# Optimization experiments

Measured on AMD Instinct MI355X. Metric: run time of the kernel, lower is better.

The kernel has to match this reference:

```python
import jax, jax.numpy as jnp
import numpy as np

B, T, D, U = 128, 1024, 256, 256


def setup_inputs() -> dict:
    key = jax.random.key(0)
    ks = jax.random.split(key, 16)
    s_in = 1.0 / np.sqrt(D)
    s_rec = 1.0 / np.sqrt(U)
    inp = {"x": jax.random.normal(ks[0], (B, T, D), dtype=jnp.float32)}
    for i, name in enumerate(["wf", "wi", "wc", "wo"]):
        inp[name] = jax.random.normal(ks[1 + i], (D, U), dtype=jnp.float32) * s_in
    for i, name in enumerate(["rf", "ri", "rc", "ro", "pf", "pi", "po"]):
        inp[name] = jax.random.normal(ks[5 + i], (U, U), dtype=jnp.float32) * s_rec
    for i, name in enumerate(["bf", "bi", "bc", "bo"]):
        inp[name] = jax.random.normal(ks[12 + i], (U,), dtype=jnp.float32) * 0.01
    return inp


def reference(x, wf, wi, wc, wo, rf, ri, rc, ro, pf, pi, po, bf, bi, bc, bo):
    # Peephole LSTM: scan over time, state (c, h) each [B, U].
    def step(carry, xt):
        c, h = carry
        f_gate = jax.nn.sigmoid(xt @ wf + h @ rf + c @ pf + bf)
        i_gate = jax.nn.sigmoid(xt @ wi + h @ ri + c @ pi + bi)
        c_tild = jnp.tanh(xt @ wc + h @ rc + bc)
        c_new = f_gate * c + i_gate * c_tild
        o_gate = jax.nn.sigmoid(xt @ wo + h @ ro + c_new @ po + bo)
        h_new = jnp.tanh(c_new) * o_gate
        return (c_new, h_new), None

    b = x.shape[0]
    u = wf.shape[1]
    c0 = jnp.zeros((b, u), dtype=x.dtype)
    h0 = jnp.zeros((b, u), dtype=x.dtype)
    (_, h_final), _ = jax.lax.scan(step, (c0, h0), jnp.swapaxes(x, 0, 1))  # time-major [T,B,D]
    return h_final
```

## Files before the change

kernel.cpp:

```cpp
#include <hip/hip_runtime.h>

#define TT 1024
#define DU 256

#define CEX_OFF   0
#define HEX_OFF   65536
#define STMP_OFF  131072
#define TST_OFF   139264
#define GCON_OFF  172032
#define BLOB_OFF  174080
#define CHUNK_ELEMS (11*16*256)

typedef unsigned short ushort_t;
typedef unsigned u32;
typedef unsigned long long u64;
typedef __attribute__((ext_vector_type(8))) short short8;
typedef __attribute__((ext_vector_type(2))) unsigned long long u64x2;
typedef __attribute__((ext_vector_type(4))) float floatx4;

#define MFMA(a, b, c) __builtin_amdgcn_mfma_f32_16x16x32_bf16((a), (b), (c), 0, 0, 0)

__device__ __forceinline__ ushort_t f2bf(float f) {
  unsigned u = __float_as_uint(f);
  return (ushort_t)((u + 0x7fffu + ((u >> 16) & 1u)) >> 16);
}
__device__ __forceinline__ float sigf(float x) { return 1.0f / (1.0f + __expf(-x)); }
__device__ __forceinline__ float tanhf_(float x) {
  float t = 1.0f - 2.0f / (__expf(2.0f * fabsf(x)) + 1.0f);
  return copysignf(t, x);
}

__device__ __forceinline__ short8 ldfrag(const ushort_t* p) {
  union { struct { u64 a, b; } q; short8 s; } v;
  v.q.a = __hip_atomic_load((const u64*)p,       __ATOMIC_RELAXED, __HIP_MEMORY_SCOPE_AGENT);
  v.q.b = __hip_atomic_load((const u64*)(p + 4), __ATOMIC_RELAXED, __HIP_MEMORY_SCOPE_AGENT);
  return v.s;
}
__device__ __forceinline__ void wait_half_slow(const u32* stG, u32 tgt, int lane, int wv) {
  const u32* p = stG + (wv * 8 + (lane & 7)) * 2 + ((lane >> 3) & 1);
  for (;;) {
    u32 s = __hip_atomic_load(p, __ATOMIC_RELAXED, __HIP_MEMORY_SCOPE_AGENT);
    if (__all((int)(s >= tgt))) return;
    __builtin_amdgcn_s_sleep(1);
  }
}

__device__ __forceinline__ u32 poll_nt(const u32* p) {
  u32 s;
  asm volatile("global_load_dword %0, %1, off nt\n\ts_waitcnt vmcnt(0)"
               : "=v"(s) : "v"(p) : "memory");
  return s;
}
__device__ __forceinline__ int wait_half_f(const u32* stG, u32 tgt, int lane, int wv) {
  const u32* p = stG + (wv * 8 + (lane & 7)) * 2 + ((lane >> 3) & 1);
  int it = 0;
  for (;;) {
    u32 s = poll_nt(p);
    if (__all((int)(s >= tgt))) return 1;
    if (++it > 16384) return 0;
  }
}
__device__ __forceinline__ short8 ldfrag_nt(const ushort_t* p) {
  union { u64x2 q; short8 s; } v;
  v.q = __builtin_nontemporal_load((const u64x2*)p);
  return v.s;
}

__device__ int test_nt(u32* tb, int mem, int lane) {
  u64* td = (u64*)tb;
  u32* tstamp = tb + 256;
  u32* tready = tb + 512;
  int ok = 1;
  for (int r = 0; r < 3; ++r) {
    u32 seq = 1u + (u32)r;
    if (lane == 0)
      __hip_atomic_store(tready + mem, seq, __ATOMIC_RELEASE, __HIP_MEMORY_SCOPE_AGENT);
    { int it = 0;
      for (;;) {
        u32 v = __hip_atomic_load(tready + (lane & 15), __ATOMIC_RELAXED,
                                  __HIP_MEMORY_SCOPE_AGENT);
        if (__all((int)(v >= seq))) break;
        if (++it > 16384) return 0;
        __builtin_amdgcn_s_sleep(2);
      } }
    if (lane < 8) {
      u64 v = 0x9E3779B97F4A7C15ull * (u64)(seq * 131u + (u32)mem * 17u + (u32)lane + 1u);
      asm volatile("global_store_dwordx2 %0, %1, off"
                   :: "v"(td + mem * 8 + lane), "v"(v) : "memory");
    }
    asm volatile("s_waitcnt vmcnt(0)" ::: "memory");
    if (lane == 0)
      asm volatile("global_store_dword %0, %1, off"
                   :: "v"(tstamp + mem * 16), "v"(seq) : "memory");
    int saw = 0;
    { int it = 0;
      for (;;) {
        u32 s = poll_nt(tstamp + (lane & 15) * 16);
        if (__all((int)(s >= seq))) { saw = 1; break; }
        if (++it > 192) break;
        __builtin_amdgcn_s_sleep(2);
      } }
    if (!saw) { ok = 0; continue; }
    u64 a = __builtin_nontemporal_load(td + lane);
    u64 b = __builtin_nontemporal_load(td + lane + 64);
    int s0 = lane >> 3, j0 = lane & 7, s1 = (lane + 64) >> 3, j1 = (lane + 64) & 7;
    u64 e0 = 0x9E3779B97F4A7C15ull * (u64)(seq * 131u + (u32)s0 * 17u + (u32)j0 + 1u);
    u64 e1 = 0x9E3779B97F4A7C15ull * (u64)(seq * 131u + (u32)s1 * 17u + (u32)j1 + 1u);
    if (!__all((int)((a == e0) && (b == e1)))) ok = 0;
  }
  return ok;
}

__global__ void conv_weights(
    const float* __restrict__ wf, const float* __restrict__ wi,
    const float* __restrict__ wc, const float* __restrict__ wo,
    const float* __restrict__ rf, const float* __restrict__ ri,
    const float* __restrict__ rc, const float* __restrict__ ro,
    const float* __restrict__ pf, const float* __restrict__ pi,
    const float* __restrict__ po, ushort_t* __restrict__ blob)
{
  int id = blockIdx.x * 256 + threadIdx.x;
  int k   = id & 255;
  int col = (id >> 8) & 15;
  int q   = id >> 12;
  int m   = q % 11;
  int mm  = q / 11;
  const float* srcs[11] = {wf, wi, wc, wo, rf, ri, rc, ro, pf, pi, po};
  float v = srcs[m][k * 256 + mm * 16 + col];
  unsigned u = __float_as_uint(v);
  blob[id] = (ushort_t)((u + 0x7fffu + ((u >> 16) & 1u)) >> 16);
}

extern "C" __global__ void __launch_bounds__(128, 1)
lstm_rec(const float* __restrict__ x, const ushort_t* __restrict__ blob,
         ushort_t* __restrict__ h_ex, ushort_t* __restrict__ c_ex,
         u32* __restrict__ stamps, u32* __restrict__ tst, u32* __restrict__ gcon,
         const float* __restrict__ bfv, const float* __restrict__ biv,
         const float* __restrict__ bcv, const float* __restrict__ bov,
         float* __restrict__ out)
{
  __shared__ ushort_t xa[16 * 264];
  __shared__ float pre2[2][4][16][17];
  __shared__ float pop2[2][16][17];
  __shared__ float bia[4][16];
  __shared__ int s_mode;

  const int tid = threadIdx.x;
  const int bid = blockIdx.x;
  const int wv = tid >> 6;
  const int lane = tid & 63;
  const int lr = lane & 15;
  const int lk = lane >> 4;

  const int grp = bid & 7;
  const int mem = bid >> 3;
  const int gb0 = grp * 16;
  const int gc0 = mem * 16;

  u32* gok  = gcon;
  u32* gpol = gcon + 256;

  if (wv == 0) {
    __builtin_amdgcn_fence(__ATOMIC_ACQUIRE, "agent");
    int okv = test_nt(tst + grp * 1024, mem, lane);
    if (lane == 0)
      __hip_atomic_store(gok + bid, 1u | ((u32)okv << 1),
                         __ATOMIC_RELEASE, __HIP_MEMORY_SCOPE_AGENT);
    if (bid == 0) {
      u32 pol = 0; int it = 0;
      for (;;) {
        u32 a = __hip_atomic_load(gok + lane, __ATOMIC_RELAXED, __HIP_MEMORY_SCOPE_AGENT);
        u32 b = __hip_atomic_load(gok + 64 + lane, __ATOMIC_RELAXED, __HIP_MEMORY_SCOPE_AGENT);
        if (__all((int)((a & 1u) && (b & 1u)))) {
          pol = __all((int)(((a >> 1) & 1u) && ((b >> 1) & 1u))) ? 1u : 0u;
          break;
        }
        if (++it > 32768) { pol = 0; break; }
        __builtin_amdgcn_s_sleep(4);
      }
      if (lane == 0)
        __hip_atomic_store(gpol, pol + 1u, __ATOMIC_RELEASE, __HIP_MEMORY_SCOPE_AGENT);
    }
    u32 p;
    for (;;) {
      p = __hip_atomic_load(gpol, __ATOMIC_RELAXED, __HIP_MEMORY_SCOPE_AGENT);
      if (p) break;
      __builtin_amdgcn_s_sleep(4);
    }
    if (lane == 0) s_mode = (int)(p - 1u);
  }
  __syncthreads();
  const int mode = s_mode;
  int wedged = 0;
  if (mode) __builtin_amdgcn_fence(__ATOMIC_ACQUIRE, "agent");

  const ushort_t* wb = blob + (size_t)mem * CHUNK_ELEMS;
  short8 wW[4][4], wR[4][4], wPf[4], wPi[4], wPo[4];
#pragma unroll
  for (int s = 0; s < 4; ++s) {
    const int ko = wv * 128 + s * 32 + lk * 8;
#pragma unroll
    for (int g = 0; g < 4; ++g) {
      wW[g][s] = *(const short8*)(wb + ((g    ) * 16 + lr) * 256 + ko);
      wR[g][s] = *(const short8*)(wb + ((4 + g) * 16 + lr) * 256 + ko);
    }
    wPf[s] = *(const short8*)(wb + (8  * 16 + lr) * 256 + ko);
    wPi[s] = *(const short8*)(wb + (9  * 16 + lr) * 256 + ko);
    wPo[s] = *(const short8*)(wb + (10 * 16 + lr) * 256 + ko);
  }

  if (tid < 64) {
    const float* bs = (tid < 16) ? bfv : (tid < 32) ? biv : (tid < 48) ? bcv : bov;
    bia[tid >> 4][tid & 15] = bs[gc0 + (tid & 15)];
  }
  const int pb = tid >> 3, pc = (tid & 7) * 2;
  float cr0 = 0.f, cr1 = 0.f;

  const int xr = tid >> 3, xc = (tid & 7) * 32;
  {
    const float* xp = x + (size_t)(gb0 + xr) * TT * DU + xc;
#pragma unroll
    for (int u = 0; u < 8; ++u) {
      float4 f = *(const float4*)(xp + u * 4);
      *(u64*)&xa[xr * 264 + xc + u * 4] =
          (u64)f2bf(f.x) | ((u64)f2bf(f.y) << 16) |
          ((u64)f2bf(f.z) << 32) | ((u64)f2bf(f.w) << 48);
    }
  }
  __syncthreads();

  const floatx4 z4 = {0.f, 0.f, 0.f, 0.f};
  floatx4 acc[4] = {z4, z4, z4, z4};
#pragma unroll
  for (int s = 0; s < 4; ++s) {
    int k = wv * 128 + s * 32 + lk * 8;
    short8 a = *(const short8*)&xa[lr * 264 + k];
    acc[0] = MFMA(a, wW[0][s], acc[0]);
    acc[1] = MFMA(a, wW[1][s], acc[1]);
    acc[2] = MFMA(a, wW[2][s], acc[2]);
    acc[3] = MFMA(a, wW[3][s], acc[3]);
  }

  u32* stG = stamps + grp * 32;
  ushort_t* cG = c_ex + grp * 16 * 256;
  ushort_t* hG = h_ex + grp * 16 * 256;
  u32* cSlot = (u32*)(cG + mem * 256 + pb * 16 + pc);
  u32* hSlot = (u32*)(hG + mem * 256 + pb * 16 + pc);
  u32* mySt  = stG + mem * 2 + wv;

  for (int t = 0; t < TT; ++t) {
    if (t > 0) {
      if (mode) { if (!wedged && !wait_half_f(stG, 2u * (u32)t, lane, wv)) wedged = 1; }
      else wait_half_slow(stG, 2u * (u32)t, lane, wv);
      short8 hf[4];
#pragma unroll
      for (int s = 0; s < 4; ++s) {
        int k = wv * 128 + s * 32 + lk * 8;
        hf[s] = mode ? ldfrag_nt(hG + (k >> 4) * 256 + lr * 16 + (k & 15))
                     : ldfrag(hG + (k >> 4) * 256 + lr * 16 + (k & 15));
      }
#pragma unroll
      for (int s = 0; s < 4; ++s) {
        acc[0] = MFMA(hf[s], wR[0][s], acc[0]);
        acc[1] = MFMA(hf[s], wR[1][s], acc[1]);
        acc[2] = MFMA(hf[s], wR[2][s], acc[2]);
        acc[3] = MFMA(hf[s], wR[3][s], acc[3]);
      }
    }
#pragma unroll
    for (int g = 0; g < 4; ++g)
#pragma unroll
      for (int r = 0; r < 4; ++r)
        pre2[wv][g][lk * 4 + r][lr] = acc[g][r];
    __syncthreads();

    {
      float fg = sigf(pre2[0][0][pb][pc] + pre2[1][0][pb][pc] + bia[0][pc]);
      float ig = sigf(pre2[0][1][pb][pc] + pre2[1][1][pb][pc] + bia[1][pc]);
      float ct = tanhf_(pre2[0][2][pb][pc] + pre2[1][2][pb][pc] + bia[2][pc]);
      cr0 = fg * cr0 + ig * ct;
      fg = sigf(pre2[0][0][pb][pc + 1] + pre2[1][0][pb][pc + 1] + bia[0][pc + 1]);
      ig = sigf(pre2[0][1][pb][pc + 1] + pre2[1][1][pb][pc + 1] + bia[1][pc + 1]);
      ct = tanhf_(pre2[0][2][pb][pc + 1] + pre2[1][2][pb][pc + 1] + bia[2][pc + 1]);
      cr1 = fg * cr1 + ig * ct;
    }
    {
      u32 cw = (u32)f2bf(cr0) | ((u32)f2bf(cr1) << 16);
      if (mode)
        asm volatile("global_store_dword %0, %1, off" :: "v"(cSlot), "v"(cw) : "memory");
      else
        __hip_atomic_store(cSlot, cw, __ATOMIC_RELAXED, __HIP_MEMORY_SCOPE_AGENT);
      asm volatile("s_waitcnt vmcnt(0)" ::: "memory");
      if (lane == 0) {
        u32 sv = 2u * (u32)t + 1u;
        if (mode)
          asm volatile("global_store_dword %0, %1, off" :: "v"(mySt), "v"(sv) : "memory");
        else
          __hip_atomic_store(mySt, sv, __ATOMIC_RELAXED, __HIP_MEMORY_SCOPE_AGENT);
      }
    }

    if (t < TT - 1) {
      float4 xf[8];
      const float* xp = x + ((size_t)(gb0 + xr) * TT + (t + 1)) * DU + xc;
#pragma unroll
      for (int u = 0; u < 8; ++u) xf[u] = *(const float4*)(xp + u * 4);
#pragma unroll
      for (int u = 0; u < 8; ++u) {
        float4 f = xf[u];
        *(u64*)&xa[xr * 264 + xc + u * 4] =
            (u64)f2bf(f.x) | ((u64)f2bf(f.y) << 16) |
            ((u64)f2bf(f.z) << 32) | ((u64)f2bf(f.w) << 48);
      }
      __syncthreads();
    }

    if (mode) { if (!wedged && !wait_half_f(stG, 2u * (u32)t + 1u, lane, wv)) wedged = 1; }
    else wait_half_slow(stG, 2u * (u32)t + 1u, lane, wv);

    short8 cf[4];
#pragma unroll
    for (int s = 0; s < 4; ++s) {
      int k = wv * 128 + s * 32 + lk * 8;
      cf[s] = mode ? ldfrag_nt(cG + (k >> 4) * 256 + lr * 16 + (k & 15))
                   : ldfrag(cG + (k >> 4) * 256 + lr * 16 + (k & 15));
    }
    {
      floatx4 pacc = z4;
#pragma unroll
      for (int s = 0; s < 4; ++s) pacc = MFMA(cf[s], wPo[s], pacc);
#pragma unroll
      for (int r = 0; r < 4; ++r) pop2[wv][lk * 4 + r][lr] = pacc[r];
    }
    __syncthreads();

    float og0 = sigf(pre2[0][3][pb][pc] + pre2[1][3][pb][pc]
                   + pop2[0][pb][pc] + pop2[1][pb][pc] + bia[3][pc]);
    float hv0 = tanhf_(cr0) * og0;
    float og1 = sigf(pre2[0][3][pb][pc + 1] + pre2[1][3][pb][pc + 1]
                   + pop2[0][pb][pc + 1] + pop2[1][pb][pc + 1] + bia[3][pc + 1]);
    float hv1 = tanhf_(cr1) * og1;
    if (t == TT - 1) {
      float2 o2; o2.x = hv0; o2.y = hv1;
      *(float2*)&out[(gb0 + pb) * 256 + gc0 + pc] = o2;
      break;
    }
    {
      u32 hw = (u32)f2bf(hv0) | ((u32)f2bf(hv1) << 16);
      if (mode)
        asm volatile("global_store_dword %0, %1, off" :: "v"(hSlot), "v"(hw) : "memory");
      else
        __hip_atomic_store(hSlot, hw, __ATOMIC_RELAXED, __HIP_MEMORY_SCOPE_AGENT);
      asm volatile("s_waitcnt vmcnt(0)" ::: "memory");
      if (lane == 0) {
        u32 sv = 2u * (u32)t + 2u;
        if (mode)
          asm volatile("global_store_dword %0, %1, off" :: "v"(mySt), "v"(sv) : "memory");
        else
          __hip_atomic_store(mySt, sv, __ATOMIC_RELAXED, __HIP_MEMORY_SCOPE_AGENT);
      }
    }

#pragma unroll
    for (int g = 0; g < 4; ++g) acc[g] = z4;
#pragma unroll
    for (int s = 0; s < 4; ++s) {
      int k = wv * 128 + s * 32 + lk * 8;
      short8 a = *(const short8*)&xa[lr * 264 + k];
      acc[0] = MFMA(a, wW[0][s], acc[0]);
      acc[1] = MFMA(a, wW[1][s], acc[1]);
      acc[2] = MFMA(a, wW[2][s], acc[2]);
      acc[3] = MFMA(a, wW[3][s], acc[3]);
    }
#pragma unroll
    for (int s = 0; s < 4; ++s) {
      acc[0] = MFMA(cf[s], wPf[s], acc[0]);
      acc[1] = MFMA(cf[s], wPi[s], acc[1]);
    }
  }
}

extern "C" void kernel_launch(void* const* d_in, const int* in_sizes, int n_in,
                              void* d_out, int out_size, void* d_ws, size_t ws_size,
                              hipStream_t stream) {
  const float* x   = (const float*)d_in[0];
  const float* bfv = (const float*)d_in[12];
  const float* biv = (const float*)d_in[13];
  const float* bcv = (const float*)d_in[14];
  const float* bov = (const float*)d_in[15];
  float* outp = (float*)d_out;

  char* ws = (char*)d_ws;
  ushort_t* c_exp = (ushort_t*)(ws + CEX_OFF);
  ushort_t* h_exp = (ushort_t*)(ws + HEX_OFF);
  u32* stmp = (u32*)(ws + STMP_OFF);
  u32* tstp = (u32*)(ws + TST_OFF);
  u32* gcon = (u32*)(ws + GCON_OFF);
  ushort_t* blob = (ushort_t*)(ws + BLOB_OFF);

  hipMemsetAsync(d_ws, 0, BLOB_OFF, stream);

  hipLaunchKernelGGL(conv_weights, dim3(2816), dim3(256), 0, stream,
                     (const float*)d_in[1], (const float*)d_in[2],
                     (const float*)d_in[3], (const float*)d_in[4],
                     (const float*)d_in[5], (const float*)d_in[6],
                     (const float*)d_in[7], (const float*)d_in[8],
                     (const float*)d_in[9], (const float*)d_in[10],
                     (const float*)d_in[11], blob);

  hipLaunchKernelGGL(lstm_rec, dim3(128), dim3(128), 0, stream,
                     x, (const ushort_t*)blob, h_exp, c_exp, stmp, tstp, gcon,
                     bfv, biv, bcv, bov, outp);
}
```

Before: 3.001 ms.

## Replace stamp-based sync with tagged data words polled directly

Each published h/c word is now packed with its timestep tag into a 64-bit slot, so consumers poll the data itself instead of first waiting on per-wave stamps and then loading. This removes the store→waitcnt→stamp-store round trip on the producer side and a separate stamp poll plus data load on the consumer side per half-step. The pre-activation shared buffer is double-buffered by timestep parity. The cost is twice the exchange traffic per poll, and correctness relies on each 64-bit store landing atomically.

Result: slower. 3.692 ms (+23.0%).

```diff
diff --git a/kernel.cpp b/kernel.cpp
--- a/kernel.cpp
+++ b/kernel.cpp
@@ -4,11 +4,10 @@
 #define DU 256
 
 #define CEX_OFF   0
-#define HEX_OFF   65536
-#define STMP_OFF  131072
-#define TST_OFF   139264
-#define GCON_OFF  172032
-#define BLOB_OFF  174080
+#define HEX_OFF   131072
+#define TST_OFF   262144
+#define GCON_OFF  294912
+#define BLOB_OFF  296960
 #define CHUNK_ELEMS (11*16*256)
 
 typedef unsigned short ushort_t;
@@ -30,42 +29,78 @@
   return copysignf(t, x);
 }
 
-__device__ __forceinline__ short8 ldfrag(const ushort_t* p) {
-  union { struct { u64 a, b; } q; short8 s; } v;
-  v.q.a = __hip_atomic_load((const u64*)p,       __ATOMIC_RELAXED, __HIP_MEMORY_SCOPE_AGENT);
-  v.q.b = __hip_atomic_load((const u64*)(p + 4), __ATOMIC_RELAXED, __HIP_MEMORY_SCOPE_AGENT);
-  return v.s;
-}
-__device__ __forceinline__ void wait_half_slow(const u32* stG, u32 tgt, int lane, int wv) {
-  const u32* p = stG + (wv * 8 + (lane & 7)) * 2 + ((lane >> 3) & 1);
+
+__device__ __forceinline__ void pub_tagged(u64* slot, u32 data, u32 tag, int mode) {
+  u64 v = ((u64)tag << 32) | (u64)data;
+  if (mode)
+    asm volatile("global_store_dwordx2 %0, %1, off" :: "v"(slot), "v"(v) : "memory");
+  else
+    __hip_atomic_store(slot, v, __ATOMIC_RELAXED, __HIP_MEMORY_SCOPE_AGENT);
+}
+
+__device__ __forceinline__ int poll_frags_fast(const u64* ex, u32 tag,
+                                               int wv, int lr, int lk, short8 fr[4]) {
+  u64x2 q[4][2];
+  int it = 0, done = 1;
   for (;;) {
-    u32 s = __hip_atomic_load(p, __ATOMIC_RELAXED, __HIP_MEMORY_SCOPE_AGENT);
-    if (__all((int)(s >= tgt))) return;
+    int ok = 1;
+#pragma unroll
+    for (int s = 0; s < 4; ++s) {
+      int k = wv * 128 + s * 32 + lk * 8;
+      const u64* p = ex + ((k >> 4) * 128 + lr * 8 + ((k & 15) >> 1));
+      asm volatile("global_load_dwordx4 %0, %2, off nt\n\t"
+                   "global_load_dwordx4 %1, %3, off nt\n\t"
+                   "s_waitcnt vmcnt(0)"
+                   : "=v"(q[s][0]), "=v"(q[s][1])
+                   : "v"(p), "v"(p + 2) : "memory");
+      ok &= (int)(((u32)(q[s][0][0] >> 32) == tag) & ((u32)(q[s][0][1] >> 32) == tag) &
+                  ((u32)(q[s][1][0] >> 32) == tag) & ((u32)(q[s][1][1] >> 32) == tag));
+    }
+    if (__all(ok)) break;
+    if (++it > 16384) { done = 0; break; }
+  }
+#pragma unroll
+  for (int s = 0; s < 4; ++s) {
+    union { u32 w[4]; short8 s8; } u;
+    u.w[0] = (u32)q[s][0][0]; u.w[1] = (u32)q[s][0][1];
+    u.w[2] = (u32)q[s][1][0]; u.w[3] = (u32)q[s][1][1];
+    fr[s] = u.s8;
+  }
+  return done;
+}
+__device__ __forceinline__ void poll_frags_slow(const u64* ex, u32 tag,
+                                                int wv, int lr, int lk, short8 fr[4]) {
+  u64 q[4][4];
+  for (;;) {
+    int ok = 1;
+#pragma unroll
+    for (int s = 0; s < 4; ++s) {
+      int k = wv * 128 + s * 32 + lk * 8;
+      const u64* p = ex + ((k >> 4) * 128 + lr * 8 + ((k & 15) >> 1));
+#pragma unroll
+      for (int j = 0; j < 4; ++j) {
+        q[s][j] = __hip_atomic_load(p + j, __ATOMIC_RELAXED, __HIP_MEMORY_SCOPE_AGENT);
+        ok &= (int)((u32)(q[s][j] >> 32) == tag);
+      }
+    }
+    if (__all(ok)) break;
     __builtin_amdgcn_s_sleep(1);
   }
-}
-
-__device__ __forceinline__ u32 poll_nt(const u32* p) {
+#pragma unroll
+  for (int s = 0; s < 4; ++s) {
+    union { u32 w[4]; short8 s8; } u;
+#pragma unroll
+    for (int j = 0; j < 4; ++j) u.w[j] = (u32)q[s][j];
+    fr[s] = u.s8;
+  }
+}
+
+__device__ __forceinline__ u32 poll_nt1(const u32* p) {
   u32 s;
   asm volatile("global_load_dword %0, %1, off nt\n\ts_waitcnt vmcnt(0)"
                : "=v"(s) : "v"(p) : "memory");
   return s;
 }
-__device__ __forceinline__ int wait_half_f(const u32* stG, u32 tgt, int lane, int wv) {
-  const u32* p = stG + (wv * 8 + (lane & 7)) * 2 + ((lane >> 3) & 1);
-  int it = 0;
-  for (;;) {
-    u32 s = poll_nt(p);
-    if (__all((int)(s >= tgt))) return 1;
-    if (++it > 16384) return 0;
-  }
-}
-__device__ __forceinline__ short8 ldfrag_nt(const ushort_t* p) {
-  union { u64x2 q; short8 s; } v;
-  v.q = __builtin_nontemporal_load((const u64x2*)p);
-  return v.s;
-}
-
 __device__ int test_nt(u32* tb, int mem, int lane) {
   u64* td = (u64*)tb;
   u32* tstamp = tb + 256;
@@ -95,7 +130,7 @@
     int saw = 0;
     { int it = 0;
       for (;;) {
-        u32 s = poll_nt(tstamp + (lane & 15) * 16);
+        u32 s = poll_nt1(tstamp + (lane & 15) * 16);
         if (__all((int)(s >= seq))) { saw = 1; break; }
         if (++it > 192) break;
         __builtin_amdgcn_s_sleep(2);
@@ -133,14 +168,14 @@
 
 extern "C" __global__ void __launch_bounds__(128, 1)
 lstm_rec(const float* __restrict__ x, const ushort_t* __restrict__ blob,
-         ushort_t* __restrict__ h_ex, ushort_t* __restrict__ c_ex,
-         u32* __restrict__ stamps, u32* __restrict__ tst, u32* __restrict__ gcon,
+         u64* __restrict__ h_ex, u64* __restrict__ c_ex,
+         u32* __restrict__ tst, u32* __restrict__ gcon,
          const float* __restrict__ bfv, const float* __restrict__ biv,
          const float* __restrict__ bcv, const float* __restrict__ bov,
          float* __restrict__ out)
 {
   __shared__ ushort_t xa[16 * 264];
-  __shared__ float pre2[2][4][16][17];
+  __shared__ float pre2[2][2][4][16][17];
   __shared__ float pop2[2][16][17];
   __shared__ float bia[4][16];
   __shared__ int s_mode;
@@ -241,24 +276,17 @@
     acc[3] = MFMA(a, wW[3][s], acc[3]);
   }
 
-  u32* stG = stamps + grp * 32;
-  ushort_t* cG = c_ex + grp * 16 * 256;
-  ushort_t* hG = h_ex + grp * 16 * 256;
-  u32* cSlot = (u32*)(cG + mem * 256 + pb * 16 + pc);
-  u32* hSlot = (u32*)(hG + mem * 256 + pb * 16 + pc);
-  u32* mySt  = stG + mem * 2 + wv;
+  u64* cG = c_ex + grp * 16 * 128;
+  u64* hG = h_ex + grp * 16 * 128;
+  u64* cSlot = cG + mem * 128 + pb * 8 + (tid & 7);
+  u64* hSlot = hG + mem * 128 + pb * 8 + (tid & 7);
 
   for (int t = 0; t < TT; ++t) {
+    const int tp = t & 1;
     if (t > 0) {
-      if (mode) { if (!wedged && !wait_half_f(stG, 2u * (u32)t, lane, wv)) wedged = 1; }
-      else wait_half_slow(stG, 2u * (u32)t, lane, wv);
       short8 hf[4];
-#pragma unroll
-      for (int s = 0; s < 4; ++s) {
-        int k = wv * 128 + s * 32 + lk * 8;
-        hf[s] = mode ? ldfrag_nt(hG + (k >> 4) * 256 + lr * 16 + (k & 15))
-                     : ldfrag(hG + (k >> 4) * 256 + lr * 16 + (k & 15));
-      }
+      if (mode) { if (!poll_frags_fast(hG, (u32)t, wv, lr, lk, hf) && !wedged) wedged = 1; }
+      else poll_frags_slow(hG, (u32)t, wv, lr, lk, hf);
 #pragma unroll
       for (int s = 0; s < 4; ++s) {
         acc[0] = MFMA(hf[s], wR[0][s], acc[0]);
@@ -271,34 +299,20 @@
     for (int g = 0; g < 4; ++g)
 #pragma unroll
       for (int r = 0; r < 4; ++r)
-        pre2[wv][g][lk * 4 + r][lr] = acc[g][r];
+        pre2[tp][wv][g][lk * 4 + r][lr] = acc[g][r];
     __syncthreads();
 
     {
-      float fg = sigf(pre2[0][0][pb][pc] + pre2[1][0][pb][pc] + bia[0][pc]);
-      float ig = sigf(pre2[0][1][pb][pc] + pre2[1][1][pb][pc] + bia[1][pc]);
-      float ct = tanhf_(pre2[0][2][pb][pc] + pre2[1][2][pb][pc] + bia[2][pc]);
+      float fg = sigf(pre2[tp][0][0][pb][pc] + pre2[tp][1][0][pb][pc] + bia[0][pc]);
+      float ig = sigf(pre2[tp][0][1][pb][pc] + pre2[tp][1][1][pb][pc] + bia[1][pc]);
+      float ct = tanhf_(pre2[tp][0][2][pb][pc] + pre2[tp][1][2][pb][pc] + bia[2][pc]);
       cr0 = fg * cr0 + ig * ct;
-      fg = sigf(pre2[0][0][pb][pc + 1] + pre2[1][0][pb][pc + 1] + bia[0][pc + 1]);
-      ig = sigf(pre2[0][1][pb][pc + 1] + pre2[1][1][pb][pc + 1] + bia[1][pc + 1]);
-      ct = tanhf_(pre2[0][2][pb][pc + 1] + pre2[1][2][pb][pc + 1] + bia[2][pc + 1]);
+      fg = sigf(pre2[tp][0][0][pb][pc + 1] + pre2[tp][1][0][pb][pc + 1] + bia[0][pc + 1]);
+      ig = sigf(pre2[tp][0][1][pb][pc + 1] + pre2[tp][1][1][pb][pc + 1] + bia[1][pc + 1]);
+      ct = tanhf_(pre2[tp][0][2][pb][pc + 1] + pre2[tp][1][2][pb][pc + 1] + bia[2][pc + 1]);
       cr1 = fg * cr1 + ig * ct;
     }
-    {
-      u32 cw = (u32)f2bf(cr0) | ((u32)f2bf(cr1) << 16);
-      if (mode)
-        asm volatile("global_store_dword %0, %1, off" :: "v"(cSlot), "v"(cw) : "memory");
-      else
-        __hip_atomic_store(cSlot, cw, __ATOMIC_RELAXED, __HIP_MEMORY_SCOPE_AGENT);
-      asm volatile("s_waitcnt vmcnt(0)" ::: "memory");
-      if (lane == 0) {
-        u32 sv = 2u * (u32)t + 1u;
-        if (mode)
-          asm volatile("global_store_dword %0, %1, off" :: "v"(mySt), "v"(sv) : "memory");
-        else
-          __hip_atomic_store(mySt, sv, __ATOMIC_RELAXED, __HIP_MEMORY_SCOPE_AGENT);
-      }
-    }
+    pub_tagged(cSlot, (u32)f2bf(cr0) | ((u32)f2bf(cr1) << 16), (u32)t + 1u, mode);
 
     if (t < TT - 1) {
       float4 xf[8];
@@ -315,16 +329,9 @@
       __syncthreads();
     }
 
-    if (mode) { if (!wedged && !wait_half_f(stG, 2u * (u32)t + 1u, lane, wv)) wedged = 1; }
-    else wait_half_slow(stG, 2u * (u32)t + 1u, lane, wv);
-
     short8 cf[4];
-#pragma unroll
-    for (int s = 0; s < 4; ++s) {
-      int k = wv * 128 + s * 32 + lk * 8;
-      cf[s] = mode ? ldfrag_nt(cG + (k >> 4) * 256 + lr * 16 + (k & 15))
-                   : ldfrag(cG + (k >> 4) * 256 + lr * 16 + (k & 15));
-    }
+    if (mode) { if (!poll_frags_fast(cG, (u32)t + 1u, wv, lr, lk, cf) && !wedged) wedged = 1; }
+    else poll_frags_slow(cG, (u32)t + 1u, wv, lr, lk, cf);
     {
       floatx4 pacc = z4;
 #pragma unroll
@@ -334,10 +341,10 @@
     }
     __syncthreads();
 
-    float og0 = sigf(pre2[0][3][pb][pc] + pre2[1][3][pb][pc]
+    float og0 = sigf(pre2[tp][0][3][pb][pc] + pre2[tp][1][3][pb][pc]
                    + pop2[0][pb][pc] + pop2[1][pb][pc] + bia[3][pc]);
     float hv0 = tanhf_(cr0) * og0;
-    float og1 = sigf(pre2[0][3][pb][pc + 1] + pre2[1][3][pb][pc + 1]
+    float og1 = sigf(pre2[tp][0][3][pb][pc + 1] + pre2[tp][1][3][pb][pc + 1]
                    + pop2[0][pb][pc + 1] + pop2[1][pb][pc + 1] + bia[3][pc + 1]);
     float hv1 = tanhf_(cr1) * og1;
     if (t == TT - 1) {
@@ -345,21 +352,7 @@
       *(float2*)&out[(gb0 + pb) * 256 + gc0 + pc] = o2;
       break;
     }
-    {
-      u32 hw = (u32)f2bf(hv0) | ((u32)f2bf(hv1) << 16);
-      if (mode)
-        asm volatile("global_store_dword %0, %1, off" :: "v"(hSlot), "v"(hw) : "memory");
-      else
-        __hip_atomic_store(hSlot, hw, __ATOMIC_RELAXED, __HIP_MEMORY_SCOPE_AGENT);
-      asm volatile("s_waitcnt vmcnt(0)" ::: "memory");
-      if (lane == 0) {
-        u32 sv = 2u * (u32)t + 2u;
-        if (mode)
-          asm volatile("global_store_dword %0, %1, off" :: "v"(mySt), "v"(sv) : "memory");
-        else
-          __hip_atomic_store(mySt, sv, __ATOMIC_RELAXED, __HIP_MEMORY_SCOPE_AGENT);
-      }
-    }
+    pub_tagged(hSlot, (u32)f2bf(hv0) | ((u32)f2bf(hv1) << 16), (u32)t + 1u, mode);
 
 #pragma unroll
     for (int g = 0; g < 4; ++g) acc[g] = z4;
@@ -391,9 +384,8 @@
   float* outp = (float*)d_out;
 
   char* ws = (char*)d_ws;
-  ushort_t* c_exp = (ushort_t*)(ws + CEX_OFF);
-  ushort_t* h_exp = (ushort_t*)(ws + HEX_OFF);
-  u32* stmp = (u32*)(ws + STMP_OFF);
+  u64* c_exp = (u64*)(ws + CEX_OFF);
+  u64* h_exp = (u64*)(ws + HEX_OFF);
   u32* tstp = (u32*)(ws + TST_OFF);
   u32* gcon = (u32*)(ws + GCON_OFF);
   ushort_t* blob = (ushort_t*)(ws + BLOB_OFF);
@@ -409,6 +401,6 @@
                      (const float*)d_in[11], blob);
 
   hipLaunchKernelGGL(lstm_rec, dim3(128), dim3(128), 0, stream,
-                     x, (const ushort_t*)blob, h_exp, c_exp, stmp, tstp, gcon,
+                     x, (const ushort_t*)blob, h_exp, c_exp, tstp, gcon,
                      bfv, biv, bcv, bov, outp);
 }
```
